# Optimization experiments

Hardware: AMD Instinct MI355X
Metric: run time of the kernel (lower is better)

## Reference

```python
import jax, jax.numpy as jnp
import numpy as np

NEG_SLOPE = 0.2
N_NODES = 50000
N_EDGES = 800000


def gat_conv(h, src, dst, W, al, ar, residual):
    """One DGL-style GATConv layer. h: [N, F_in]; returns [N, H*D]."""
    N = h.shape[0]
    H, D = al.shape
    feat = (h @ W).reshape(N, H, D)                 # [N, H, D]
    el = jnp.sum(feat * al, axis=-1)                # [N, H]
    er = jnp.sum(feat * ar, axis=-1)                # [N, H]
    e = jax.nn.leaky_relu(el[src] + er[dst], NEG_SLOPE)   # [E, H]
    # segment softmax over incoming edges of each destination node
    emax = jax.ops.segment_max(e, dst, num_segments=N)    # [N, H]
    ex = jnp.exp(e - emax[dst])                           # [E, H]
    denom = jax.ops.segment_sum(ex, dst, num_segments=N)  # [N, H]
    a = ex / denom[dst]                                   # [E, H]
    msg = feat[src] * a[:, :, None]                       # [E, H, D]
    rst = jax.ops.segment_sum(msg, dst, num_segments=N)   # [N, H, D]
    if residual:  # identity residual: in_feats == H*D
        rst = rst + h.reshape(N, H, D)
    return jax.nn.elu(rst).reshape(N, H * D)


def setup_inputs() -> dict:
    key = jax.random.key(0)
    ks = jax.random.split(key, 9)
    features = jax.random.normal(ks[0], (N_NODES, 256), dtype=jnp.float32)
    src = jax.random.randint(ks[1], (N_EDGES,), 0, N_NODES, dtype=jnp.int32)
    dst = jax.random.randint(ks[2], (N_EDGES,), 0, N_NODES, dtype=jnp.int32)
    s1 = 1.0 / np.sqrt(256.0)
    W1 = jax.random.normal(ks[3], (256, 256), dtype=jnp.float32) * s1
    al1 = jax.random.normal(ks[4], (4, 64), dtype=jnp.float32) * 0.1
    ar1 = jax.random.normal(ks[5], (4, 64), dtype=jnp.float32) * 0.1
    W2 = jax.random.normal(ks[6], (256, 256), dtype=jnp.float32) * s1
    al2 = jax.random.normal(ks[7], (4, 64), dtype=jnp.float32) * 0.1
    ar2 = jax.random.normal(ks[8], (4, 64), dtype=jnp.float32) * 0.1
    return {"features": features, "src": src, "dst": dst,
            "W1": W1, "al1": al1, "ar1": ar1,
            "W2": W2, "al2": al2, "ar2": ar2}


def reference(features, src, dst, W1, al1, ar1, W2, al2, ar2):
    h = gat_conv(features, src, dst, W1, al1, ar1, residual=False)
    h = gat_conv(h, src, dst, W2, al2, ar2, residual=True)
    return h  # [N, 256]
```

## Files before the change

kernel.cpp:

```cpp
#include <hip/hip_runtime.h>
#include <hip/hip_bf16.h>

#define N_NODES 50000
#define N_EDGES 800000
#define NHEAD 4
#define DHEAD 64
#define FDIM 256
#define SCANB 1024
#define NSCAN ((N_NODES + SCANB - 1) / SCANB)

typedef __attribute__((ext_vector_type(8))) short bfrag8;
typedef __attribute__((ext_vector_type(4))) float f32x4;

__device__ __forceinline__ unsigned f2bf_rne(float x) {
    unsigned u = __float_as_uint(x);
    return (u + 0x7fffu + ((u >> 16) & 1u)) >> 16;
}
__device__ __forceinline__ float bf2f(unsigned u) {
    return __uint_as_float(u << 16);
}

__global__ void degree_kernel(const int* __restrict__ dst, int* __restrict__ cnt, int E) {
    int e = blockIdx.x * 256 + threadIdx.x;
    if (e < E) atomicAdd(&cnt[dst[e]], 1);
}

__global__ __launch_bounds__(1024) void scan1_kernel(const int* __restrict__ cnt,
                                                     int* __restrict__ partial,
                                                     int* __restrict__ bsum, int N) {
    __shared__ int sdata[SCANB];
    int i = blockIdx.x * SCANB + (int)threadIdx.x;
    int v = (i < N) ? cnt[i] : 0;
    sdata[threadIdx.x] = v;
    __syncthreads();
    for (int off = 1; off < SCANB; off <<= 1) {
        int t = (threadIdx.x >= (unsigned)off) ? sdata[threadIdx.x - off] : 0;
        __syncthreads();
        sdata[threadIdx.x] += t;
        __syncthreads();
    }
    if (i < N) partial[i] = sdata[threadIdx.x];
    if (threadIdx.x == SCANB - 1) bsum[blockIdx.x] = sdata[SCANB - 1];
}

__global__ void scan2_kernel(const int* __restrict__ bsum, int* __restrict__ boff, int nb) {
    int lane = threadIdx.x;
    int v = (lane < nb) ? bsum[lane] : 0;
#pragma unroll
    for (int off = 1; off < 64; off <<= 1) {
        int o = __shfl_up(v, off, 64);
        if (lane >= off) v += o;
    }
    int excl = __shfl_up(v, 1, 64);
    if (lane == 0) excl = 0;
    if (lane < nb) boff[lane] = excl;
}

__global__ __launch_bounds__(1024) void scan3_kernel(const int* __restrict__ partial,
                                                     const int* __restrict__ boff,
                                                     int* __restrict__ rowptr,
                                                     int* __restrict__ cursor, int N) {
    int i = blockIdx.x * SCANB + (int)threadIdx.x;
    if (i < N) {
        int inc = partial[i] + boff[blockIdx.x];
        rowptr[i + 1] = inc;
        if (i + 1 < N) cursor[i + 1] = inc;
    }
    if (i == 0) { rowptr[0] = 0; cursor[0] = 0; }
}

__global__ void scatter_kernel(const int* __restrict__ src, const int* __restrict__ dst,
                               int* __restrict__ cursor, int* __restrict__ srcs, int E) {
    int e = blockIdx.x * 256 + threadIdx.x;
    if (e < E) {
        int pos = atomicAdd(&cursor[dst[e]], 1);
        srcs[pos] = src[e];
    }
}

__global__ __launch_bounds__(256) void bconv_kernel(const float* __restrict__ B,
                                                    ushort* __restrict__ Bth,
                                                    ushort* __restrict__ Btl) {
    __shared__ ushort th[16][264], tl[16][264];
    int k0 = blockIdx.x * 16;
    int n = threadIdx.x;
#pragma unroll
    for (int k = 0; k < 16; ++k) {
        float v = B[(size_t)(k0 + k) * 256 + n];
        unsigned hb = f2bf_rne(v);
        th[k][n] = (ushort)hb;
        tl[k][n] = (ushort)(__float_as_uint(v - bf2f(hb)) >> 16);
    }
    __syncthreads();
    ushort oh[16], ol[16];
#pragma unroll
    for (int k = 0; k < 16; ++k) { oh[k] = th[k][n]; ol[k] = tl[k][n]; }
#pragma unroll
    for (int q = 0; q < 4; ++q) {
        *reinterpret_cast<ushort4*>(Bth + (size_t)n * 256 + k0 + q * 4) =
            make_ushort4(oh[q*4+0], oh[q*4+1], oh[q*4+2], oh[q*4+3]);
        *reinterpret_cast<ushort4*>(Btl + (size_t)n * 256 + k0 + q * 4) =
            make_ushort4(ol[q*4+0], ol[q*4+1], ol[q*4+2], ol[q*4+3]);
    }
}

template <int SPLITA>
__global__ __launch_bounds__(256) void gemm_mfma_kernel(const float* __restrict__ Af,
                                                        const ushort* __restrict__ Ahg,
                                                        const ushort* __restrict__ Bth,
                                                        const ushort* __restrict__ Btl,
                                                        ushort* __restrict__ Cb, int M) {
    __shared__ ushort Ah[128][40];
    __shared__ ushort Bh[128][40], Bl[128][40];
    const int t = threadIdx.x;
    const int lane = t & 63, wave = t >> 6;
    const int wr = wave >> 1, wc = wave & 1;
    const int row0 = blockIdx.x * 128;
    const int col0 = blockIdx.y * 128;

    f32x4 acc[4][4];
#pragma unroll
    for (int i = 0; i < 4; ++i)
#pragma unroll
        for (int j = 0; j < 4; ++j) { acc[i][j].x = 0.f; acc[i][j].y = 0.f; acc[i][j].z = 0.f; acc[i][j].w = 0.f; }

    const int srow = t >> 1;
    const int skoff = (t & 1) * 16;
    int arow = row0 + srow; if (arow >= M) arow = M - 1;
    const size_t abase = (size_t)arow * 256 + skoff;
    const size_t bbase = (size_t)(col0 + srow) * 256 + skoff;

    float4 af0, af1, af2, af3;
    uint4 r0, r1;
    uint4 r4, r5, r6, r7;

#define LOADK(kk)                                                              \
    do {                                                                       \
        if constexpr (SPLITA) {                                                \
            const float4* pa = reinterpret_cast<const float4*>(Af + abase + (kk)); \
            af0 = pa[0]; af1 = pa[1]; af2 = pa[2]; af3 = pa[3];                \
        } else {                                                               \
            r0 = *reinterpret_cast<const uint4*>(Ahg + abase + (kk));          \
            r1 = *reinterpret_cast<const uint4*>(Ahg + abase + (kk) + 8);      \
        }                                                                      \
        r4 = *reinterpret_cast<const uint4*>(Bth + bbase + (kk));              \
        r5 = *reinterpret_cast<const uint4*>(Bth + bbase + (kk) + 8);          \
        r6 = *reinterpret_cast<const uint4*>(Btl + bbase + (kk));              \
        r7 = *reinterpret_cast<const uint4*>(Btl + bbase + (kk) + 8);          \
    } while (0)

    LOADK(0);
#pragma unroll
    for (int kk = 0; kk < 256; kk += 32) {
        if (kk) __syncthreads();
        if constexpr (SPLITA) {
            float v[16];
            v[0]=af0.x; v[1]=af0.y; v[2]=af0.z; v[3]=af0.w;
            v[4]=af1.x; v[5]=af1.y; v[6]=af1.z; v[7]=af1.w;
            v[8]=af2.x; v[9]=af2.y; v[10]=af2.z; v[11]=af2.w;
            v[12]=af3.x; v[13]=af3.y; v[14]=af3.z; v[15]=af3.w;
            ushort hh[16];
#pragma unroll
            for (int q = 0; q < 16; ++q) hh[q] = (ushort)f2bf_rne(v[q]);
#pragma unroll
            for (int q = 0; q < 4; ++q) {
                *reinterpret_cast<ushort4*>(&Ah[srow][skoff + q * 4]) =
                    make_ushort4(hh[q*4+0], hh[q*4+1], hh[q*4+2], hh[q*4+3]);
            }
        } else {
            *reinterpret_cast<uint4*>(&Ah[srow][skoff])     = r0;
            *reinterpret_cast<uint4*>(&Ah[srow][skoff + 8]) = r1;
        }
        *reinterpret_cast<uint4*>(&Bh[srow][skoff])     = r4;
        *reinterpret_cast<uint4*>(&Bh[srow][skoff + 8]) = r5;
        *reinterpret_cast<uint4*>(&Bl[srow][skoff])     = r6;
        *reinterpret_cast<uint4*>(&Bl[srow][skoff + 8]) = r7;
        __syncthreads();
        if (kk + 32 < 256) LOADK(kk + 32);

        const int kg = (lane >> 4) * 8;
        const int rsel = lane & 15;
        bfrag8 afh[4], bfh[4], bfl[4];
#pragma unroll
        for (int i = 0; i < 4; ++i)
            afh[i] = *reinterpret_cast<const bfrag8*>(&Ah[wr * 64 + i * 16 + rsel][kg]);
#pragma unroll
        for (int j = 0; j < 4; ++j) {
            bfh[j] = *reinterpret_cast<const bfrag8*>(&Bh[wc * 64 + j * 16 + rsel][kg]);
            bfl[j] = *reinterpret_cast<const bfrag8*>(&Bl[wc * 64 + j * 16 + rsel][kg]);
        }
#pragma unroll
        for (int i = 0; i < 4; ++i)
#pragma unroll
            for (int j = 0; j < 4; ++j) {
                acc[i][j] = __builtin_amdgcn_mfma_f32_16x16x32_bf16(afh[i], bfh[j], acc[i][j], 0, 0, 0);
                acc[i][j] = __builtin_amdgcn_mfma_f32_16x16x32_bf16(afh[i], bfl[j], acc[i][j], 0, 0, 0);
            }
    }
#undef LOADK
    const int ccol = lane & 15;
    const int crow = (lane >> 4) * 4;
#pragma unroll
    for (int i = 0; i < 4; ++i) {
#pragma unroll
        for (int r = 0; r < 4; ++r) {
            int row = row0 + wr * 64 + i * 16 + crow + r;
            if (row >= M) continue;
#pragma unroll
            for (int j = 0; j < 4; ++j) {
                int col = col0 + wc * 64 + j * 16 + ccol;
                float val = (r == 0) ? acc[i][j].x : (r == 1) ? acc[i][j].y : (r == 2) ? acc[i][j].z : acc[i][j].w;
                Cb[(size_t)row * 256 + col] = (ushort)f2bf_rne(val);
            }
        }
    }
}

__global__ void eler_kernel(const ushort* __restrict__ featb, const float* __restrict__ al,
                            const float* __restrict__ ar, float* __restrict__ el,
                            float* __restrict__ er, int N) {
    int node = blockIdx.x * 4 + (threadIdx.x >> 6);
    if (node >= N) return;
    int lane = threadIdx.x & 63;
    ushort4 fu = *reinterpret_cast<const ushort4*>(featb + (size_t)node * FDIM + lane * 4);
    float f0 = bf2f(fu.x), f1 = bf2f(fu.y), f2 = bf2f(fu.z), f3 = bf2f(fu.w);
    float4 a = *reinterpret_cast<const float4*>(al + lane * 4);
    float4 b = *reinterpret_cast<const float4*>(ar + lane * 4);
    float pl = f0 * a.x + f1 * a.y + f2 * a.z + f3 * a.w;
    float pr = f0 * b.x + f1 * b.y + f2 * b.z + f3 * b.w;
#pragma unroll
    for (int m = 1; m < 16; m <<= 1) {
        pl += __shfl_xor(pl, m, 64);
        pr += __shfl_xor(pr, m, 64);
    }
    if ((lane & 15) == 0) {
        int h = lane >> 4;
        el[node * NHEAD + h] = pl;
        er[node * NHEAD + h] = pr;
    }
}

__global__ __launch_bounds__(256) void agg_kernel(
        const ushort* __restrict__ featb, const float* __restrict__ el,
        const float* __restrict__ er, const int* __restrict__ rowptr,
        const int* __restrict__ srcs,
        const ushort* __restrict__ resid_h, const ushort* __restrict__ resid_l,
        float* __restrict__ outf, ushort* __restrict__ outh, ushort* __restrict__ outl,
        int N) {
    int node = blockIdx.x * 4 + (threadIdx.x >> 6);
    if (node >= N) return;
    int lane = threadIdx.x & 63;
    int h4 = lane & 3;
    int eo = lane >> 2;
    int head = lane >> 4;
    float erh = er[(size_t)node * NHEAD + h4];
    int beg = rowptr[node], end = rowptr[node + 1];

    float m = -1e30f, ls = 0.f;
    for (int base = beg; base < end; base += 16) {
        int p = base + eo;
        float x = -1e30f;
        if (p < end) {
            int s = srcs[p];
            float t = el[(size_t)s * NHEAD + h4] + erh;
            x = t > 0.f ? t : 0.2f * t;
        }
        float cm = x;
        cm = fmaxf(cm, __shfl_xor(cm, 4, 64));
        cm = fmaxf(cm, __shfl_xor(cm, 8, 64));
        cm = fmaxf(cm, __shfl_xor(cm, 16, 64));
        cm = fmaxf(cm, __shfl_xor(cm, 32, 64));
        float mn = fmaxf(m, cm);
        ls = ls * __expf(m - mn) + ((p < end) ? __expf(x - mn) : 0.f);
        m = mn;
    }
    ls += __shfl_xor(ls, 4, 64);
    ls += __shfl_xor(ls, 8, 64);
    ls += __shfl_xor(ls, 16, 64);
    ls += __shfl_xor(ls, 32, 64);
    float dinv = ls > 0.f ? 1.0f / ls : 0.f;

    f32x4 a0 = {0.f, 0.f, 0.f, 0.f}, a1 = a0, a2 = a0, a3 = a0;
    for (int base = beg; base < end; base += 16) {
        int p = base + eo;
        int smine = 0;
        float wmine = 0.f;
        if (p < end) {
            smine = srcs[p];
            float t = el[(size_t)smine * NHEAD + h4] + erh;
            t = t > 0.f ? t : 0.2f * t;
            wmine = __expf(t - m) * dinv;
        }
        int jmax = end - base; if (jmax > 16) jmax = 16;
        int j = 0;
        for (; j + 3 < jmax; j += 4) {
            int sl0 = 4 * j + head;
            int s0 = __shfl(smine, sl0, 64);
            int s1 = __shfl(smine, sl0 + 4, 64);
            int s2 = __shfl(smine, sl0 + 8, 64);
            int s3 = __shfl(smine, sl0 + 12, 64);
            float w0 = __shfl(wmine, sl0, 64);
            float w1 = __shfl(wmine, sl0 + 4, 64);
            float w2 = __shfl(wmine, sl0 + 8, 64);
            float w3 = __shfl(wmine, sl0 + 12, 64);
            ushort4 f0 = *reinterpret_cast<const ushort4*>(featb + (size_t)s0 * FDIM + lane * 4);
            ushort4 f1 = *reinterpret_cast<const ushort4*>(featb + (size_t)s1 * FDIM + lane * 4);
            ushort4 f2 = *reinterpret_cast<const ushort4*>(featb + (size_t)s2 * FDIM + lane * 4);
            ushort4 f3 = *reinterpret_cast<const ushort4*>(featb + (size_t)s3 * FDIM + lane * 4);
            a0.x = fmaf(w0, bf2f(f0.x), a0.x); a0.y = fmaf(w0, bf2f(f0.y), a0.y);
            a0.z = fmaf(w0, bf2f(f0.z), a0.z); a0.w = fmaf(w0, bf2f(f0.w), a0.w);
            a1.x = fmaf(w1, bf2f(f1.x), a1.x); a1.y = fmaf(w1, bf2f(f1.y), a1.y);
            a1.z = fmaf(w1, bf2f(f1.z), a1.z); a1.w = fmaf(w1, bf2f(f1.w), a1.w);
            a2.x = fmaf(w2, bf2f(f2.x), a2.x); a2.y = fmaf(w2, bf2f(f2.y), a2.y);
            a2.z = fmaf(w2, bf2f(f2.z), a2.z); a2.w = fmaf(w2, bf2f(f2.w), a2.w);
            a3.x = fmaf(w3, bf2f(f3.x), a3.x); a3.y = fmaf(w3, bf2f(f3.y), a3.y);
            a3.z = fmaf(w3, bf2f(f3.z), a3.z); a3.w = fmaf(w3, bf2f(f3.w), a3.w);
        }
        for (; j < jmax; ++j) {
            int sl = 4 * j + head;
            int s0 = __shfl(smine, sl, 64);
            float w0 = __shfl(wmine, sl, 64);
            ushort4 f0 = *reinterpret_cast<const ushort4*>(featb + (size_t)s0 * FDIM + lane * 4);
            a0.x = fmaf(w0, bf2f(f0.x), a0.x); a0.y = fmaf(w0, bf2f(f0.y), a0.y);
            a0.z = fmaf(w0, bf2f(f0.z), a0.z); a0.w = fmaf(w0, bf2f(f0.w), a0.w);
        }
    }
    float4 acc = make_float4(a0.x + a1.x + a2.x + a3.x, a0.y + a1.y + a2.y + a3.y,
                             a0.z + a1.z + a2.z + a3.z, a0.w + a1.w + a2.w + a3.w);

    if (resid_h) {
        ushort4 rh = *reinterpret_cast<const ushort4*>(resid_h + (size_t)node * FDIM + lane * 4);
        ushort4 rl = *reinterpret_cast<const ushort4*>(resid_l + (size_t)node * FDIM + lane * 4);
        acc.x += bf2f(rh.x) + bf2f(rl.x);
        acc.y += bf2f(rh.y) + bf2f(rl.y);
        acc.z += bf2f(rh.z) + bf2f(rl.z);
        acc.w += bf2f(rh.w) + bf2f(rl.w);
    }
    acc.x = acc.x > 0.f ? acc.x : expm1f(acc.x);
    acc.y = acc.y > 0.f ? acc.y : expm1f(acc.y);
    acc.z = acc.z > 0.f ? acc.z : expm1f(acc.z);
    acc.w = acc.w > 0.f ? acc.w : expm1f(acc.w);

    if (outf) {
        *reinterpret_cast<float4*>(outf + (size_t)node * FDIM + lane * 4) = acc;
    } else {
        unsigned h0 = f2bf_rne(acc.x), h1 = f2bf_rne(acc.y), h2 = f2bf_rne(acc.z), h3 = f2bf_rne(acc.w);
        *reinterpret_cast<ushort4*>(outh + (size_t)node * FDIM + lane * 4) =
            make_ushort4((ushort)h0, (ushort)h1, (ushort)h2, (ushort)h3);
        *reinterpret_cast<ushort4*>(outl + (size_t)node * FDIM + lane * 4) = make_ushort4(
            (ushort)(__float_as_uint(acc.x - bf2f(h0)) >> 16),
            (ushort)(__float_as_uint(acc.y - bf2f(h1)) >> 16),
            (ushort)(__float_as_uint(acc.z - bf2f(h2)) >> 16),
            (ushort)(__float_as_uint(acc.w - bf2f(h3)) >> 16));
    }
}

extern "C" void kernel_launch(void* const* d_in, const int* in_sizes, int n_in,
                              void* d_out, int out_size, void* d_ws, size_t ws_size,
                              hipStream_t stream) {
    const float* features = (const float*)d_in[0];
    const int*   src      = (const int*)d_in[1];
    const int*   dst      = (const int*)d_in[2];
    const float* W1       = (const float*)d_in[3];
    const float* al1      = (const float*)d_in[4];
    const float* ar1      = (const float*)d_in[5];
    const float* W2       = (const float*)d_in[6];
    const float* al2      = (const float*)d_in[7];
    const float* ar2      = (const float*)d_in[8];
    float* out = (float*)d_out;

    const int N = N_NODES, E = N_EDGES;

    char* ws = (char*)d_ws;
    size_t off = 0;
    auto alloc = [&](size_t bytes) -> void* {
        void* p = ws + off;
        off = (off + bytes + 255) & ~(size_t)255;
        return p;
    };
    ushort* featb  = (ushort*)alloc((size_t)N * FDIM * 2);
    ushort* Afh    = (ushort*)alloc((size_t)N * FDIM * 2);
    ushort* Afl    = (ushort*)alloc((size_t)N * FDIM * 2);
    float*  el     = (float*)alloc((size_t)N * NHEAD * 4);
    float*  er     = (float*)alloc((size_t)N * NHEAD * 4);
    int*    rowptr = (int*)alloc((size_t)(N + 1) * 4);
    int*    cnt    = (int*)alloc((size_t)N * 4);
    int*    cursor = (int*)alloc((size_t)N * 4);
    int*    partial= (int*)alloc((size_t)N * 4);
    int*    bsum   = (int*)alloc((size_t)NSCAN * 4);
    int*    boff   = (int*)alloc((size_t)NSCAN * 4);
    int*    srcs   = (int*)alloc((size_t)E * 4);
    ushort* Bth    = (ushort*)alloc((size_t)256 * 256 * 2);
    ushort* Btl    = (ushort*)alloc((size_t)256 * 256 * 2);

    const int egrid = (E + 255) / 256;
    const int ngrid4 = (N + 3) / 4;

    hipMemsetAsync(cnt, 0, (size_t)N * 4, stream);
    degree_kernel<<<egrid, 256, 0, stream>>>(dst, cnt, E);
    scan1_kernel<<<NSCAN, SCANB, 0, stream>>>(cnt, partial, bsum, N);
    scan2_kernel<<<1, 64, 0, stream>>>(bsum, boff, NSCAN);
    scan3_kernel<<<NSCAN, SCANB, 0, stream>>>(partial, boff, rowptr, cursor, N);
    scatter_kernel<<<egrid, 256, 0, stream>>>(src, dst, cursor, srcs, E);

    dim3 ggrid((N + 127) / 128, 2);

    bconv_kernel<<<16, 256, 0, stream>>>(W1, Bth, Btl);
    gemm_mfma_kernel<1><<<ggrid, 256, 0, stream>>>(features, nullptr, Bth, Btl, featb, N);
    eler_kernel<<<ngrid4, 256, 0, stream>>>(featb, al1, ar1, el, er, N);
    agg_kernel<<<ngrid4, 256, 0, stream>>>(featb, el, er, rowptr, srcs,
                                           nullptr, nullptr, nullptr, Afh, Afl, N);

    bconv_kernel<<<16, 256, 0, stream>>>(W2, Bth, Btl);
    gemm_mfma_kernel<0><<<ggrid, 256, 0, stream>>>(nullptr, Afh, Bth, Btl, featb, N);
    eler_kernel<<<ngrid4, 256, 0, stream>>>(featb, al2, ar2, el, er, N);
    agg_kernel<<<ngrid4, 256, 0, stream>>>(featb, el, er, rowptr, srcs,
                                           Afh, Afl, out, nullptr, nullptr, N);
}
```

Before: 321.6 us.

## Fuse attention logits into GEMM epilogue and drop split-bf16 weight correction

Computes el/er directly in the GEMM epilogue from the fp32 accumulators, using shuffles across the 16-column groups, so the separate eler kernels and their feature re-reads go away. The weight matrix is no longer split into high and low bf16 halves, which halves the B-side MFMA work, LDS traffic and loads. Both weight conversions now run in a single launch. This lowers GEMM precision, and el/er are now computed from fp32 accumulators rather than from rounded bf16 features.

```diff
diff --git a/kernel.cpp b/kernel.cpp
--- a/kernel.cpp
+++ b/kernel.cpp
@@ -78,40 +78,40 @@
     }
 }
 
-__global__ __launch_bounds__(256) void bconv_kernel(const float* __restrict__ B,
-                                                    ushort* __restrict__ Bth,
-                                                    ushort* __restrict__ Btl) {
-    __shared__ ushort th[16][264], tl[16][264];
+__global__ __launch_bounds__(256) void bconv_kernel(const float* __restrict__ B1,
+                                                    const float* __restrict__ B2,
+                                                    ushort* __restrict__ Bt1,
+                                                    ushort* __restrict__ Bt2) {
+    const float* B = blockIdx.y ? B2 : B1;
+    ushort* Bt = blockIdx.y ? Bt2 : Bt1;
+    __shared__ ushort th[16][264];
     int k0 = blockIdx.x * 16;
     int n = threadIdx.x;
 #pragma unroll
-    for (int k = 0; k < 16; ++k) {
-        float v = B[(size_t)(k0 + k) * 256 + n];
-        unsigned hb = f2bf_rne(v);
-        th[k][n] = (ushort)hb;
-        tl[k][n] = (ushort)(__float_as_uint(v - bf2f(hb)) >> 16);
-    }
+    for (int k = 0; k < 16; ++k)
+        th[k][n] = (ushort)f2bf_rne(B[(size_t)(k0 + k) * 256 + n]);
     __syncthreads();
-    ushort oh[16], ol[16];
-#pragma unroll
-    for (int k = 0; k < 16; ++k) { oh[k] = th[k][n]; ol[k] = tl[k][n]; }
-#pragma unroll
-    for (int q = 0; q < 4; ++q) {
-        *reinterpret_cast<ushort4*>(Bth + (size_t)n * 256 + k0 + q * 4) =
+    ushort oh[16];
+#pragma unroll
+    for (int k = 0; k < 16; ++k) oh[k] = th[k][n];
+#pragma unroll
+    for (int q = 0; q < 4; ++q)
+        *reinterpret_cast<ushort4*>(Bt1 == Bt ? Bt1 + (size_t)n * 256 + k0 + q * 4
+                                              : Bt2 + (size_t)n * 256 + k0 + q * 4) =
             make_ushort4(oh[q*4+0], oh[q*4+1], oh[q*4+2], oh[q*4+3]);
-        *reinterpret_cast<ushort4*>(Btl + (size_t)n * 256 + k0 + q * 4) =
-            make_ushort4(ol[q*4+0], ol[q*4+1], ol[q*4+2], ol[q*4+3]);
-    }
 }
 
 template <int SPLITA>
 __global__ __launch_bounds__(256) void gemm_mfma_kernel(const float* __restrict__ Af,
                                                         const ushort* __restrict__ Ahg,
-                                                        const ushort* __restrict__ Bth,
-                                                        const ushort* __restrict__ Btl,
-                                                        ushort* __restrict__ Cb, int M) {
+                                                        const ushort* __restrict__ Bt,
+                                                        ushort* __restrict__ Cb,
+                                                        const float* __restrict__ al,
+                                                        const float* __restrict__ ar,
+                                                        float* __restrict__ el,
+                                                        float* __restrict__ er, int M) {
     __shared__ ushort Ah[128][40];
-    __shared__ ushort Bh[128][40], Bl[128][40];
+    __shared__ ushort Bh[128][40];
     const int t = threadIdx.x;
     const int lane = t & 63, wave = t >> 6;
     const int wr = wave >> 1, wc = wave & 1;
@@ -132,7 +132,7 @@
 
     float4 af0, af1, af2, af3;
     uint4 r0, r1;
-    uint4 r4, r5, r6, r7;
+    uint4 r4, r5;
 
 #define LOADK(kk)                                                              \
     do {                                                                       \
@@ -143,10 +143,8 @@
             r0 = *reinterpret_cast<const uint4*>(Ahg + abase + (kk));          \
             r1 = *reinterpret_cast<const uint4*>(Ahg + abase + (kk) + 8);      \
         }                                                                      \
-        r4 = *reinterpret_cast<const uint4*>(Bth + bbase + (kk));              \
-        r5 = *reinterpret_cast<const uint4*>(Bth + bbase + (kk) + 8);          \
-        r6 = *reinterpret_cast<const uint4*>(Btl + bbase + (kk));              \
-        r7 = *reinterpret_cast<const uint4*>(Btl + bbase + (kk) + 8);          \
+        r4 = *reinterpret_cast<const uint4*>(Bt + bbase + (kk));               \
+        r5 = *reinterpret_cast<const uint4*>(Bt + bbase + (kk) + 8);           \
     } while (0)
 
     LOADK(0);
@@ -163,80 +161,76 @@
 #pragma unroll
             for (int q = 0; q < 16; ++q) hh[q] = (ushort)f2bf_rne(v[q]);
 #pragma unroll
-            for (int q = 0; q < 4; ++q) {
+            for (int q = 0; q < 4; ++q)
                 *reinterpret_cast<ushort4*>(&Ah[srow][skoff + q * 4]) =
                     make_ushort4(hh[q*4+0], hh[q*4+1], hh[q*4+2], hh[q*4+3]);
-            }
         } else {
             *reinterpret_cast<uint4*>(&Ah[srow][skoff])     = r0;
             *reinterpret_cast<uint4*>(&Ah[srow][skoff + 8]) = r1;
         }
         *reinterpret_cast<uint4*>(&Bh[srow][skoff])     = r4;
         *reinterpret_cast<uint4*>(&Bh[srow][skoff + 8]) = r5;
-        *reinterpret_cast<uint4*>(&Bl[srow][skoff])     = r6;
-        *reinterpret_cast<uint4*>(&Bl[srow][skoff + 8]) = r7;
         __syncthreads();
         if (kk + 32 < 256) LOADK(kk + 32);
 
         const int kg = (lane >> 4) * 8;
         const int rsel = lane & 15;
-        bfrag8 afh[4], bfh[4], bfl[4];
+        bfrag8 afh[4], bfh[4];
 #pragma unroll
         for (int i = 0; i < 4; ++i)
             afh[i] = *reinterpret_cast<const bfrag8*>(&Ah[wr * 64 + i * 16 + rsel][kg]);
 #pragma unroll
-        for (int j = 0; j < 4; ++j) {
+        for (int j = 0; j < 4; ++j)
             bfh[j] = *reinterpret_cast<const bfrag8*>(&Bh[wc * 64 + j * 16 + rsel][kg]);
-            bfl[j] = *reinterpret_cast<const bfrag8*>(&Bl[wc * 64 + j * 16 + rsel][kg]);
-        }
 #pragma unroll
         for (int i = 0; i < 4; ++i)
 #pragma unroll
-            for (int j = 0; j < 4; ++j) {
+            for (int j = 0; j < 4; ++j)
                 acc[i][j] = __builtin_amdgcn_mfma_f32_16x16x32_bf16(afh[i], bfh[j], acc[i][j], 0, 0, 0);
-                acc[i][j] = __builtin_amdgcn_mfma_f32_16x16x32_bf16(afh[i], bfl[j], acc[i][j], 0, 0, 0);
-            }
     }
 #undef LOADK
+
     const int ccol = lane & 15;
     const int crow = (lane >> 4) * 4;
+    const int head = (col0 >> 6) + wc;
+    float alv[4], arv[4];
+#pragma unroll
+    for (int j = 0; j < 4; ++j) {
+        alv[j] = al[head * 64 + j * 16 + ccol];
+        arv[j] = ar[head * 64 + j * 16 + ccol];
+    }
 #pragma unroll
     for (int i = 0; i < 4; ++i) {
 #pragma unroll
         for (int r = 0; r < 4; ++r) {
             int row = row0 + wr * 64 + i * 16 + crow + r;
-            if (row >= M) continue;
+            float vj[4];
+#pragma unroll
+            for (int j = 0; j < 4; ++j)
+                vj[j] = (r == 0) ? acc[i][j].x : (r == 1) ? acc[i][j].y : (r == 2) ? acc[i][j].z : acc[i][j].w;
+            float pl = 0.f, pr = 0.f;
 #pragma unroll
             for (int j = 0; j < 4; ++j) {
-                int col = col0 + wc * 64 + j * 16 + ccol;
-                float val = (r == 0) ? acc[i][j].x : (r == 1) ? acc[i][j].y : (r == 2) ? acc[i][j].z : acc[i][j].w;
-                Cb[(size_t)row * 256 + col] = (ushort)f2bf_rne(val);
+                pl = fmaf(vj[j], alv[j], pl);
+                pr = fmaf(vj[j], arv[j], pr);
             }
-        }
-    }
-}
-
-__global__ void eler_kernel(const ushort* __restrict__ featb, const float* __restrict__ al,
-                            const float* __restrict__ ar, float* __restrict__ el,
-                            float* __restrict__ er, int N) {
-    int node = blockIdx.x * 4 + (threadIdx.x >> 6);
-    if (node >= N) return;
-    int lane = threadIdx.x & 63;
-    ushort4 fu = *reinterpret_cast<const ushort4*>(featb + (size_t)node * FDIM + lane * 4);
-    float f0 = bf2f(fu.x), f1 = bf2f(fu.y), f2 = bf2f(fu.z), f3 = bf2f(fu.w);
-    float4 a = *reinterpret_cast<const float4*>(al + lane * 4);
-    float4 b = *reinterpret_cast<const float4*>(ar + lane * 4);
-    float pl = f0 * a.x + f1 * a.y + f2 * a.z + f3 * a.w;
-    float pr = f0 * b.x + f1 * b.y + f2 * b.z + f3 * b.w;
-#pragma unroll
-    for (int m = 1; m < 16; m <<= 1) {
-        pl += __shfl_xor(pl, m, 64);
-        pr += __shfl_xor(pr, m, 64);
-    }
-    if ((lane & 15) == 0) {
-        int h = lane >> 4;
-        el[node * NHEAD + h] = pl;
-        er[node * NHEAD + h] = pr;
+#pragma unroll
+            for (int msk = 1; msk < 16; msk <<= 1) {
+                pl += __shfl_xor(pl, msk, 64);
+                pr += __shfl_xor(pr, msk, 64);
+            }
+            if (row < M) {
+                if (ccol == 0) {
+                    el[(size_t)row * NHEAD + head] = pl;
+                    er[(size_t)row * NHEAD + head] = pr;
+                }
+#pragma unroll
+                for (int j = 0; j < 4; ++j) {
+                    int col = col0 + wc * 64 + j * 16 + ccol;
+                    Cb[(size_t)row * 256 + col] = (ushort)f2bf_rne(vj[j]);
+                }
+            }
+        }
     }
 }
 
@@ -390,8 +384,8 @@
     int*    bsum   = (int*)alloc((size_t)NSCAN * 4);
     int*    boff   = (int*)alloc((size_t)NSCAN * 4);
     int*    srcs   = (int*)alloc((size_t)E * 4);
-    ushort* Bth    = (ushort*)alloc((size_t)256 * 256 * 2);
-    ushort* Btl    = (ushort*)alloc((size_t)256 * 256 * 2);
+    ushort* Bt1    = (ushort*)alloc((size_t)256 * 256 * 2);
+    ushort* Bt2    = (ushort*)alloc((size_t)256 * 256 * 2);
 
     const int egrid = (E + 255) / 256;
     const int ngrid4 = (N + 3) / 4;
@@ -403,17 +397,17 @@
     scan3_kernel<<<NSCAN, SCANB, 0, stream>>>(partial, boff, rowptr, cursor, N);
     scatter_kernel<<<egrid, 256, 0, stream>>>(src, dst, cursor, srcs, E);
 
+    bconv_kernel<<<dim3(16, 2), 256, 0, stream>>>(W1, W2, Bt1, Bt2);
+
     dim3 ggrid((N + 127) / 128, 2);
 
-    bconv_kernel<<<16, 256, 0, stream>>>(W1, Bth, Btl);
-    gemm_mfma_kernel<1><<<ggrid, 256, 0, stream>>>(features, nullptr, Bth, Btl, featb, N);
-    eler_kernel<<<ngrid4, 256, 0, stream>>>(featb, al1, ar1, el, er, N);
+    gemm_mfma_kernel<1><<<ggrid, 256, 0, stream>>>(features, nullptr, Bt1, featb,
+                                                   al1, ar1, el, er, N);
     agg_kernel<<<ngrid4, 256, 0, stream>>>(featb, el, er, rowptr, srcs,
                                            nullptr, nullptr, nullptr, Afh, Afl, N);
 
-    bconv_kernel<<<16, 256, 0, stream>>>(W2, Bth, Btl);
-    gemm_mfma_kernel<0><<<ggrid, 256, 0, stream>>>(nullptr, Afh, Bth, Btl, featb, N);
-    eler_kernel<<<ngrid4, 256, 0, stream>>>(featb, al2, ar2, el, er, N);
+    gemm_mfma_kernel<0><<<ggrid, 256, 0, stream>>>(nullptr, Afh, Bt2, featb,
+                                                   al2, ar2, el, er, N);
     agg_kernel<<<ngrid4, 256, 0, stream>>>(featb, el, er, rowptr, srcs,
                                            Afh, Afl, out, nullptr, nullptr, N);
 }
```

Measured after the change: 304.4 us. 1.06x faster.
